# Kernel optimization log

Hardware: AMD Instinct MI355X
Metric: run time of the kernel (lower is better)

Reference implementation:

```python
import jax, jax.numpy as jnp
import numpy as np
from jax import lax

DIM = 192
HEADS = 4


def setup_inputs() -> dict:
    key = jax.random.key(0)
    ks = jax.random.split(key, 8)
    b, c, h, w = 8, DIM, 128, 128
    x = jax.random.normal(ks[0], (b, c, h, w), dtype=jnp.float32)
    Input = jax.random.normal(ks[1], (b, c, h, w), dtype=jnp.float32)
    # parameters (bias=False)
    qkv_w = jax.random.normal(ks[2], (3 * c, c), dtype=jnp.float32) * 0.02   # 1x1 conv
    dw_w = jax.random.normal(ks[3], (3 * c, 1, 3, 3), dtype=jnp.float32) * 0.02  # depthwise 3x3
    proj_w = jax.random.normal(ks[4], (c, c), dtype=jnp.float32) * 0.02      # 1x1 conv
    cm_w = jax.random.normal(ks[5], (1, c), dtype=jnp.float32) * 0.02        # changemask 1x1 conv (c -> 1)
    temperature = jnp.ones((HEADS, 1, 1), dtype=jnp.float32)
    threshold = jnp.float32(0.1)
    return {"x": x, "Input": Input, "qkv_w": qkv_w, "dw_w": dw_w,
            "proj_w": proj_w, "cm_w": cm_w, "temperature": temperature,
            "threshold": threshold}


def _l2norm(t):
    # F.normalize(dim=-1): t / max(||t||_2, eps)
    n = jnp.sqrt(jnp.sum(t * t, axis=-1, keepdims=True))
    return t / jnp.maximum(n, 1e-12)


def reference(x, Input, qkv_w, dw_w, proj_w, cm_w, temperature, threshold):
    b, c, h, w = x.shape
    # mask: threshold the residual, then a 1x1 conv to a single channel
    mask = ((Input - x) > threshold).astype(x.dtype)            # [b,c,h,w]
    mask_single = jnp.einsum('bchw,oc->bohw', mask, cm_w)        # [b,1,h,w]
    # qkv: 1x1 conv then depthwise 3x3
    qkv = jnp.einsum('bchw,oc->bohw', x, qkv_w)                  # [b,3c,h,w]
    qkv = lax.conv_general_dilated(
        qkv, dw_w, window_strides=(1, 1), padding='SAME',
        feature_group_count=3 * c,
        dimension_numbers=('NCHW', 'OIHW', 'NCHW'))
    q, k, v = jnp.split(qkv, 3, axis=1)                          # each [b,c,h,w]
    # mask repeat across channels == broadcast of single-channel mask
    q = q * mask_single
    k = k * mask_single
    ch = c // HEADS
    q = q.reshape(b, HEADS, ch, h * w)
    k = k.reshape(b, HEADS, ch, h * w)
    v = v.reshape(b, HEADS, ch, h * w)
    q = _l2norm(q)
    k = _l2norm(k)
    attn = jnp.einsum('bhcn,bhdn->bhcd', q, k) * temperature      # [b,head,ch,ch]
    attn = jax.nn.softmax(attn, axis=-1)
    out = jnp.einsum('bhcd,bhdn->bhcn', attn, v)                  # [b,head,ch,hw]
    out = out.reshape(b, c, h, w)
    out = jnp.einsum('bchw,oc->bohw', out, proj_w)                # project_out 1x1
    return out
```

## Files before the change

kernel.cpp:

```cpp
#include <hip/hip_runtime.h>
#include <hip/hip_bf16.h>

#define B 8
#define C 192
#define OC 576
#define H 128
#define W 128
#define N (H*W)
#define HEADS 4
#define CH 48

typedef __attribute__((ext_vector_type(8))) short short8;
typedef __attribute__((ext_vector_type(4))) float floatx4;

__device__ __forceinline__ float bf2f(unsigned short u) {
    union { unsigned int i; float f; } v; v.i = ((unsigned int)u) << 16; return v.f;
}
__device__ __forceinline__ unsigned short f2bf(float f) {
    __hip_bfloat16 h = (__hip_bfloat16)f;
    unsigned short u; __builtin_memcpy(&u, &h, 2); return u;
}

__global__ void k_zero(float* __restrict__ normsq, float* __restrict__ G) {
    int i = blockIdx.x * 256 + threadIdx.x;
    if (i < B * 2 * C) normsq[i] = 0.0f;
    if (i < B * HEADS * CH * CH) G[i] = 0.0f;
}

__global__ __launch_bounds__(256) void k_mask_xt(
    const float* __restrict__ x, const float* __restrict__ inp,
    const float* __restrict__ cm_w, const float* __restrict__ thr,
    float* __restrict__ mask_single, unsigned short* __restrict__ xt) {
    __shared__ unsigned short t[32][C + 2];
    __shared__ float partials[32][32];
    __shared__ float cw[C];
    int tid = threadIdx.x;
    if (tid < C) cw[tid] = cm_w[tid];
    int b = blockIdx.y, n0 = blockIdx.x * 32;
    float th = thr[0];
    const float* xb = x + (size_t)b * C * N + n0;
    const float* ib = inp + (size_t)b * C * N + n0;
    int nn4 = tid & 7;
    int c0 = tid >> 3;
    float4 xr[6], ir[6];
    #pragma unroll
    for (int it = 0; it < 6; ++it) {
        int c = c0 + it * 32;
        xr[it] = *(const float4*)&xb[(size_t)c * N + nn4 * 4];
        ir[it] = *(const float4*)&ib[(size_t)c * N + nn4 * 4];
    }
    __syncthreads();
    float s0 = 0.f, s1 = 0.f, s2 = 0.f, s3 = 0.f;
    #pragma unroll
    for (int it = 0; it < 6; ++it) {
        int c = c0 + it * 32;
        float4 xv = xr[it];
        float4 iv = ir[it];
        float wv = cw[c];
        s0 += ((iv.x - xv.x) > th) ? wv : 0.f;
        s1 += ((iv.y - xv.y) > th) ? wv : 0.f;
        s2 += ((iv.z - xv.z) > th) ? wv : 0.f;
        s3 += ((iv.w - xv.w) > th) ? wv : 0.f;
        t[nn4 * 4 + 0][c] = f2bf(xv.x);
        t[nn4 * 4 + 1][c] = f2bf(xv.y);
        t[nn4 * 4 + 2][c] = f2bf(xv.z);
        t[nn4 * 4 + 3][c] = f2bf(xv.w);
    }
    *(float4*)&partials[c0][nn4 * 4] = (float4){s0, s1, s2, s3};
    __syncthreads();
    if (tid < 32) {
        float s = 0.f;
        #pragma unroll
        for (int g = 0; g < 32; ++g) s += partials[g][tid];
        mask_single[(size_t)b * N + n0 + tid] = s;
    }
    unsigned short* db = xt + ((size_t)b * N + n0) * C;
    for (int i = tid; i < 32 * (C / 8); i += 256) {
        int r = i / (C / 8), ch = i % (C / 8);
        union { unsigned short h[8]; uint4 u; } pk;
        #pragma unroll
        for (int j = 0; j < 8; ++j) pk.h[j] = t[r][ch * 8 + j];
        *(uint4*)&db[(size_t)r * C + ch * 8] = pk.u;
    }
}

#define PAD 40
__global__ __launch_bounds__(256) void k_qkv_mfma(
    const unsigned short* __restrict__ xt, const float* __restrict__ w,
    unsigned short* __restrict__ out) {
    __shared__ __align__(16) unsigned short As[64][PAD];
    __shared__ __align__(16) unsigned short Bs[256][PAD];
    int b = blockIdx.z, m0 = blockIdx.y * 64, n0 = blockIdx.x * 256;
    int tid = threadIdx.x, wave = tid >> 6, lane = tid & 63;
    int l15 = lane & 15, quad = lane >> 4;
    floatx4 acc[4][4];
    #pragma unroll
    for (int i = 0; i < 4; ++i)
        #pragma unroll
        for (int j = 0; j < 4; ++j) acc[i][j] = (floatx4){0.f, 0.f, 0.f, 0.f};
    const unsigned short* xb = xt + (size_t)b * N * C;
    for (int k0 = 0; k0 < C; k0 += 32) {
        {
            int m = tid >> 2, ko = tid & 3;
            const float* wr = w + (size_t)(m0 + m) * C + k0 + ko * 8;
            float4 f0 = *(const float4*)&wr[0];
            float4 f1 = *(const float4*)&wr[4];
            unsigned int* dp = (unsigned int*)&As[m][ko * 8];
            dp[0] = (unsigned int)f2bf(f0.x) | ((unsigned int)f2bf(f0.y) << 16);
            dp[1] = (unsigned int)f2bf(f0.z) | ((unsigned int)f2bf(f0.w) << 16);
            dp[2] = (unsigned int)f2bf(f1.x) | ((unsigned int)f2bf(f1.y) << 16);
            dp[3] = (unsigned int)f2bf(f1.z) | ((unsigned int)f2bf(f1.w) << 16);
        }
        #pragma unroll
        for (int t = 0; t < 4; ++t) {
            int i = tid + t * 256;
            int n = i >> 2, ko = i & 3;
            *(uint4*)&Bs[n][ko * 8] = *(const uint4*)&xb[(size_t)(n0 + n) * C + k0 + ko * 8];
        }
        __syncthreads();
        short8 af[4], bf[4];
        #pragma unroll
        for (int mt = 0; mt < 4; ++mt)
            af[mt] = *(const short8*)&As[mt * 16 + l15][quad * 8];
        #pragma unroll
        for (int nt = 0; nt < 4; ++nt)
            bf[nt] = *(const short8*)&Bs[wave * 64 + nt * 16 + l15][quad * 8];
        #pragma unroll
        for (int mt = 0; mt < 4; ++mt)
            #pragma unroll
            for (int nt = 0; nt < 4; ++nt)
                acc[mt][nt] = __builtin_amdgcn_mfma_f32_16x16x32_bf16(
                    af[mt], bf[nt], acc[mt][nt], 0, 0, 0);
        __syncthreads();
    }
    unsigned short* ob = out + (size_t)b * OC * N;
    #pragma unroll
    for (int mt = 0; mt < 4; ++mt)
        #pragma unroll
        for (int r = 0; r < 4; ++r) {
            int o = m0 + mt * 16 + quad * 4 + r;
            #pragma unroll
            for (int nt = 0; nt < 4; ++nt)
                ob[(size_t)o * N + n0 + wave * 64 + nt * 16 + l15] =
                    f2bf(acc[mt][nt][r]);
        }
}

__global__ __launch_bounds__(256) void k_dwconv(
    const unsigned short* __restrict__ qkv_raw, const float* __restrict__ dw_w,
    const float* __restrict__ mask_single, unsigned short* __restrict__ qk_out,
    unsigned short* __restrict__ v_out, float* __restrict__ normsq) {
    __shared__ float tile[34][132];
    __shared__ float red[4];
    int tid = threadIdx.x;
    int b = blockIdx.z, o = blockIdx.y;
    int y0 = blockIdx.x * 32;
    const unsigned short* in = qkv_raw + ((size_t)b * OC + o) * N;
    for (int i = tid; i < 34 * 16; i += 256) {
        int r = i >> 4, dw = i & 15;
        int yy = y0 + r - 1;
        float4 f0 = {0.f, 0.f, 0.f, 0.f};
        float4 f1 = {0.f, 0.f, 0.f, 0.f};
        if (yy >= 0 && yy < H) {
            uint4 u = *(const uint4*)&in[yy * W + dw * 8];
            union { unsigned int i; float f; } a0, a1, a2, a3, a4, a5, a6, a7;
            a0.i = u.x << 16; a1.i = u.x & 0xffff0000u;
            a2.i = u.y << 16; a3.i = u.y & 0xffff0000u;
            a4.i = u.z << 16; a5.i = u.z & 0xffff0000u;
            a6.i = u.w << 16; a7.i = u.w & 0xffff0000u;
            f0.x = a0.f; f0.y = a1.f; f0.z = a2.f; f0.w = a3.f;
            f1.x = a4.f; f1.y = a5.f; f1.z = a6.f; f1.w = a7.f;
        }
        *(float4*)&tile[r][dw * 8] = f0;
        *(float4*)&tile[r][dw * 8 + 4] = f1;
        if (dw == 0)  { tile[r][130] = 0.f; tile[r][131] = 0.f; }
        if (dw == 15) { tile[r][128] = 0.f; }
    }
    __syncthreads();
    const float* wp = dw_w + o * 9;
    float w00 = wp[0], w01 = wp[1], w02 = wp[2];
    float w10 = wp[3], w11 = wp[4], w12 = wp[5];
    float w20 = wp[6], w21 = wp[7], w22 = wp[8];
    int c = tid & 63, g = tid >> 6;
    int col = c * 2;
    int lbase = (c == 0) ? 130 : (col - 2);
    bool is_qk = (o < 2 * C);
    float m_acc = 0.f;
    int rbase = g * 8;
    float2 p0l = *(const float2*)&tile[rbase][lbase];
    float2 p0m = *(const float2*)&tile[rbase][col];
    float2 p0r = *(const float2*)&tile[rbase][col + 2];
    float2 p1l = *(const float2*)&tile[rbase + 1][lbase];
    float2 p1m = *(const float2*)&tile[rbase + 1][col];
    float2 p1r = *(const float2*)&tile[rbase + 1][col + 2];
    unsigned short* qkb = qk_out + ((size_t)b * 2 * C + o) * N;
    unsigned short* vb  = v_out + ((size_t)b * C + (o - 2 * C)) * N;
    const float* mb = mask_single + (size_t)b * N;
    #pragma unroll
    for (int rl = 0; rl < 8; ++rl) {
        int tr = rbase + rl + 2;
        float2 p2l = *(const float2*)&tile[tr][lbase];
        float2 p2m = *(const float2*)&tile[tr][col];
        float2 p2r = *(const float2*)&tile[tr][col + 2];
        float sx = w00 * p0l.y + w01 * p0m.x + w02 * p0m.y
                 + w10 * p1l.y + w11 * p1m.x + w12 * p1m.y
                 + w20 * p2l.y + w21 * p2m.x + w22 * p2m.y;
        float sy = w00 * p0m.x + w01 * p0m.y + w02 * p0r.x
                 + w10 * p1m.x + w11 * p1m.y + w12 * p1r.x
                 + w20 * p2m.x + w21 * p2m.y + w22 * p2r.x;
        int p = (y0 + rbase + rl) * W + col;
        if (is_qk) {
            float2 mv = *(const float2*)&mb[p];
            sx *= mv.x; sy *= mv.y;
        }
        unsigned short hx = f2bf(sx), hy = f2bf(sy);
        unsigned int pk = (unsigned int)hx | ((unsigned int)hy << 16);
        if (is_qk) {
            *(unsigned int*)&qkb[p] = pk;
            float fx = bf2f(hx), fy = bf2f(hy);
            m_acc += fx * fx + fy * fy;
        } else {
            *(unsigned int*)&vb[p] = pk;
        }
        p0l = p1l; p0m = p1m; p0r = p1r;
        p1l = p2l; p1m = p2m; p1r = p2r;
    }
    if (is_qk) {
        #pragma unroll
        for (int off = 32; off > 0; off >>= 1) m_acc += __shfl_down(m_acc, off);
        if ((tid & 63) == 0) red[tid >> 6] = m_acc;
        __syncthreads();
        if (tid == 0)
            atomicAdd(&normsq[b * 2 * C + o], red[0] + red[1] + red[2] + red[3]);
    }
}

__global__ __launch_bounds__(256) void k_xpose_v(
    const unsigned short* __restrict__ src, unsigned short* __restrict__ dst) {
    __shared__ unsigned short t[64][C + 2];
    int tid = threadIdx.x;
    int b = blockIdx.y, n0 = blockIdx.x * 64;
    const unsigned short* sb = src + (size_t)b * C * N;
    for (int i = tid; i < C * 32; i += 256) {
        int c = i >> 5, np = i & 31;
        unsigned int u = *(const unsigned int*)&sb[(size_t)c * N + n0 + np * 2];
        t[np * 2][c] = (unsigned short)(u & 0xffffu);
        t[np * 2 + 1][c] = (unsigned short)(u >> 16);
    }
    __syncthreads();
    unsigned short* db = dst + ((size_t)b * N + n0) * C;
    for (int i = tid; i < 64 * (C / 8); i += 256) {
        int nn = i / (C / 8), ch = i % (C / 8);
        union { unsigned short h[8]; uint4 u; } pk;
        #pragma unroll
        for (int j = 0; j < 8; ++j) pk.h[j] = t[nn][ch * 8 + j];
        *(uint4*)&db[(size_t)nn * C + ch * 8] = pk.u;
    }
}

__global__ __launch_bounds__(256) void k_gram_mfma(
    const unsigned short* __restrict__ qk, float* __restrict__ G) {
    __shared__ float Gs[4][CH][CH];
    int tid = threadIdx.x, wave = tid >> 6, lane = tid & 63;
    int l15 = lane & 15, quad = lane >> 4;
    int b = blockIdx.z, hh = blockIdx.y;
    int nb = blockIdx.x * 512 + wave * 128;
    const unsigned short* qb = qk + ((size_t)b * 2 * C + hh * CH) * N;
    const unsigned short* kb = qb + (size_t)C * N;
    floatx4 acc[3][3];
    #pragma unroll
    for (int i = 0; i < 3; ++i)
        #pragma unroll
        for (int j = 0; j < 3; ++j) acc[i][j] = (floatx4){0.f, 0.f, 0.f, 0.f};
    #pragma unroll
    for (int ks = 0; ks < 4; ++ks) {
        int n_off = nb + ks * 32 + quad * 8;
        short8 af[3], bf[3];
        #pragma unroll
        for (int it = 0; it < 3; ++it)
            af[it] = *(const short8*)&qb[(size_t)(it * 16 + l15) * N + n_off];
        #pragma unroll
        for (int jt = 0; jt < 3; ++jt)
            bf[jt] = *(const short8*)&kb[(size_t)(jt * 16 + l15) * N + n_off];
        #pragma unroll
        for (int it = 0; it < 3; ++it)
            #pragma unroll
            for (int jt = 0; jt < 3; ++jt)
                acc[it][jt] = __builtin_amdgcn_mfma_f32_16x16x32_bf16(
                    af[it], bf[jt], acc[it][jt], 0, 0, 0);
    }
    #pragma unroll
    for (int it = 0; it < 3; ++it)
        #pragma unroll
        for (int jt = 0; jt < 3; ++jt)
            #pragma unroll
            for (int r = 0; r < 4; ++r)
                Gs[wave][it * 16 + quad * 4 + r][jt * 16 + l15] = acc[it][jt][r];
    __syncthreads();
    float* Gb = G + (size_t)(b * HEADS + hh) * CH * CH;
    for (int idx = tid; idx < CH * CH; idx += 256) {
        int i = idx / CH, j = idx % CH;
        atomicAdd(&Gb[idx], Gs[0][i][j] + Gs[1][i][j] + Gs[2][i][j] + Gs[3][i][j]);
    }
}

__global__ __launch_bounds__(256) void k_attn_weff(
    const float* __restrict__ G, const float* __restrict__ normsq,
    const float* __restrict__ temperature, const float* __restrict__ proj_w,
    unsigned short* __restrict__ W_eff) {
    int b = blockIdx.x;
    int o_base = blockIdx.y * 32;
    __shared__ float attn[HEADS][CH][CH];
    __shared__ float inv_n[2 * C];
    int tid = threadIdx.x;
    for (int l = tid; l < 2 * C; l += 256)
        inv_n[l] = 1.0f / fmaxf(sqrtf(normsq[b * 2 * C + l]), 1e-12f);
    __syncthreads();
    if (tid < HEADS * CH) {
        int hh = tid / CH, i = tid % CH;
        float iq = inv_n[hh * CH + i] * temperature[hh];
        const float* Gr = G + ((size_t)(b * HEADS + hh) * CH + i) * CH;
        float mx = -1e30f;
        for (int j = 0; j < CH; ++j) {
            float l2 = Gr[j] * iq * inv_n[C + hh * CH + j];
            attn[hh][i][j] = l2;
            mx = fmaxf(mx, l2);
        }
        float sm = 0.0f;
        for (int j = 0; j < CH; ++j) {
            float e = expf(attn[hh][i][j] - mx);
            attn[hh][i][j] = e;
            sm += e;
        }
        float is = 1.0f / sm;
        for (int j = 0; j < CH; ++j) attn[hh][i][j] *= is;
    }
    __syncthreads();
    for (int idx = tid; idx < 32 * C; idx += 256) {
        int o = o_base + idx / C, cp = idx % C;
        int hh = cp / CH, j = cp % CH;
        const float* pw = proj_w + (size_t)o * C + hh * CH;
        float s = 0.0f;
        #pragma unroll 8
        for (int i = 0; i < CH; ++i) s += pw[i] * attn[hh][i][j];
        W_eff[((size_t)b * C + o) * C + cp] = f2bf(s);
    }
}

__global__ __launch_bounds__(256) void k_out_mfma(
    const unsigned short* __restrict__ vt, const unsigned short* __restrict__ W_eff,
    float* __restrict__ out) {
    __shared__ __align__(16) unsigned short As[64][PAD];
    __shared__ __align__(16) unsigned short Bs[256][PAD];
    int b = blockIdx.z, m0 = blockIdx.y * 64, n0 = blockIdx.x * 256;
    int tid = threadIdx.x, wave = tid >> 6, lane = tid & 63;
    int l15 = lane & 15, quad = lane >> 4;
    floatx4 acc[4][4];
    #pragma unroll
    for (int i = 0; i < 4; ++i)
        #pragma unroll
        for (int j = 0; j < 4; ++j) acc[i][j] = (floatx4){0.f, 0.f, 0.f, 0.f};
    const unsigned short* vb = vt + (size_t)b * N * C;
    const unsigned short* wb = W_eff + (size_t)b * C * C;
    for (int k0 = 0; k0 < C; k0 += 32) {
        {
            int m = tid >> 2, ko = tid & 3;
            *(uint4*)&As[m][ko * 8] = *(const uint4*)&wb[(size_t)(m0 + m) * C + k0 + ko * 8];
        }
        #pragma unroll
        for (int t = 0; t < 4; ++t) {
            int i = tid + t * 256;
            int n = i >> 2, ko = i & 3;
            *(uint4*)&Bs[n][ko * 8] = *(const uint4*)&vb[(size_t)(n0 + n) * C + k0 + ko * 8];
        }
        __syncthreads();
        short8 af[4], bf[4];
        #pragma unroll
        for (int mt = 0; mt < 4; ++mt)
            af[mt] = *(const short8*)&As[mt * 16 + l15][quad * 8];
        #pragma unroll
        for (int nt = 0; nt < 4; ++nt)
            bf[nt] = *(const short8*)&Bs[wave * 64 + nt * 16 + l15][quad * 8];
        #pragma unroll
        for (int mt = 0; mt < 4; ++mt)
            #pragma unroll
            for (int nt = 0; nt < 4; ++nt)
                acc[mt][nt] = __builtin_amdgcn_mfma_f32_16x16x32_bf16(
                    af[mt], bf[nt], acc[mt][nt], 0, 0, 0);
        __syncthreads();
    }
    float* ob = out + (size_t)b * C * N;
    #pragma unroll
    for (int mt = 0; mt < 4; ++mt)
        #pragma unroll
        for (int r = 0; r < 4; ++r) {
            int o = m0 + mt * 16 + quad * 4 + r;
            #pragma unroll
            for (int nt = 0; nt < 4; ++nt)
                ob[(size_t)o * N + n0 + wave * 64 + nt * 16 + l15] = acc[mt][nt][r];
        }
}

extern "C" void kernel_launch(void* const* d_in, const int* in_sizes, int n_in,
                              void* d_out, int out_size, void* d_ws, size_t ws_size,
                              hipStream_t stream) {
    const float* x           = (const float*)d_in[0];
    const float* inp         = (const float*)d_in[1];
    const float* qkv_w       = (const float*)d_in[2];
    const float* dw_w        = (const float*)d_in[3];
    const float* proj_w      = (const float*)d_in[4];
    const float* cm_w        = (const float*)d_in[5];
    const float* temperature = (const float*)d_in[6];
    const float* threshold   = (const float*)d_in[7];
    float* out = (float*)d_out;

    char* ws = (char*)d_ws;
    const size_t SZ_RAW = (size_t)B * OC * N * 2;
    const size_t SZ_QK  = (size_t)B * 2 * C * N * 2;
    const size_t SZ_XT  = (size_t)B * N * C * 2;
    unsigned short* qkv_raw = (unsigned short*)ws;
    unsigned short* v_t     = (unsigned short*)ws;
    unsigned short* qk      = (unsigned short*)(ws + SZ_RAW);
    unsigned short* xt      = (unsigned short*)(ws + SZ_RAW + SZ_QK);
    unsigned short* vbuf    = xt;
    char* tail = ws + SZ_RAW + SZ_QK + SZ_XT;
    float* mask_single = (float*)tail;
    float* normsq = (float*)(tail + (size_t)B * N * 4);
    float* G = normsq + B * 2 * C;
    unsigned short* W_eff = (unsigned short*)(G + B * HEADS * CH * CH);

    k_zero<<<dim3((B * HEADS * CH * CH + 255) / 256), 256, 0, stream>>>(normsq, G);
    k_mask_xt<<<dim3(N / 32, B), 256, 0, stream>>>(x, inp, cm_w, threshold, mask_single, xt);
    k_qkv_mfma<<<dim3(N / 256, OC / 64, B), 256, 0, stream>>>(xt, qkv_w, qkv_raw);
    k_dwconv<<<dim3(H / 32, OC, B), 256, 0, stream>>>(qkv_raw, dw_w, mask_single, qk, vbuf, normsq);
    k_xpose_v<<<dim3(N / 64, B), 256, 0, stream>>>(vbuf, v_t);
    k_gram_mfma<<<dim3(N / 512, HEADS, B), 256, 0, stream>>>(qk, G);
    k_attn_weff<<<dim3(B, 6), 256, 0, stream>>>(G, normsq, temperature, proj_w, W_eff);
    k_out_mfma<<<dim3(N / 256, C / 64, B), 256, 0, stream>>>(v_t, W_eff, out);
}
```

Baseline: 509.4 us.

## Load mask/transpose tiles straight into LDS with async global_load_lds copies

The mask-and-transpose kernel now uses global-to-LDS async copies to stage fp32 x and Input tiles in shared memory, instead of loading them into registers. Each thread then reads a column of channels for one pixel, computes its share of the mask sum, and packs bf16 pairs into 16-byte stores to the transposed output. This drops the bf16 LDS transpose buffer and its second store loop, and shrinks the partial-sum reduction from 32 to 8 groups. The trade-offs are more LDS per block, which can lower occupancy, and reliance on the async copies being complete at the barrier.

```diff
diff --git a/kernel.cpp b/kernel.cpp
--- a/kernel.cpp
+++ b/kernel.cpp
@@ -21,6 +21,12 @@
     unsigned short u; __builtin_memcpy(&u, &h, 2); return u;
 }
 
+__device__ __forceinline__ void async_copy16(const float* g, float* l) {
+    __builtin_amdgcn_global_load_lds(
+        (const __attribute__((address_space(1))) unsigned int*)g,
+        (__attribute__((address_space(3))) unsigned int*)l, 16, 0, 0);
+}
+
 __global__ void k_zero(float* __restrict__ normsq, float* __restrict__ G) {
     int i = blockIdx.x * 256 + threadIdx.x;
     if (i < B * 2 * C) normsq[i] = 0.0f;
@@ -31,56 +37,50 @@
     const float* __restrict__ x, const float* __restrict__ inp,
     const float* __restrict__ cm_w, const float* __restrict__ thr,
     float* __restrict__ mask_single, unsigned short* __restrict__ xt) {
-    __shared__ unsigned short t[32][C + 2];
-    __shared__ float partials[32][32];
+    __shared__ float xs[C][32];
+    __shared__ float is_[C][32];
     __shared__ float cw[C];
+    __shared__ float partials[8][32];
     int tid = threadIdx.x;
-    if (tid < C) cw[tid] = cm_w[tid];
+    int wave = tid >> 6, lane = tid & 63;
     int b = blockIdx.y, n0 = blockIdx.x * 32;
-    float th = thr[0];
     const float* xb = x + (size_t)b * C * N + n0;
     const float* ib = inp + (size_t)b * C * N + n0;
-    int nn4 = tid & 7;
-    int c0 = tid >> 3;
-    float4 xr[6], ir[6];
-    #pragma unroll
-    for (int it = 0; it < 6; ++it) {
-        int c = c0 + it * 32;
-        xr[it] = *(const float4*)&xb[(size_t)c * N + nn4 * 4];
-        ir[it] = *(const float4*)&ib[(size_t)c * N + nn4 * 4];
-    }
-    __syncthreads();
-    float s0 = 0.f, s1 = 0.f, s2 = 0.f, s3 = 0.f;
-    #pragma unroll
-    for (int it = 0; it < 6; ++it) {
-        int c = c0 + it * 32;
-        float4 xv = xr[it];
-        float4 iv = ir[it];
-        float wv = cw[c];
-        s0 += ((iv.x - xv.x) > th) ? wv : 0.f;
-        s1 += ((iv.y - xv.y) > th) ? wv : 0.f;
-        s2 += ((iv.z - xv.z) > th) ? wv : 0.f;
-        s3 += ((iv.w - xv.w) > th) ? wv : 0.f;
-        t[nn4 * 4 + 0][c] = f2bf(xv.x);
-        t[nn4 * 4 + 1][c] = f2bf(xv.y);
-        t[nn4 * 4 + 2][c] = f2bf(xv.z);
-        t[nn4 * 4 + 3][c] = f2bf(xv.w);
-    }
-    *(float4*)&partials[c0][nn4 * 4] = (float4){s0, s1, s2, s3};
+    int cR = lane >> 3, sub = lane & 7;
+    #pragma unroll
+    for (int i = 0; i < 6; ++i) {
+        int c_base = i * 32 + wave * 8;
+        const float* gx = xb + (size_t)(c_base + cR) * N + sub * 4;
+        const float* gi = ib + (size_t)(c_base + cR) * N + sub * 4;
+        async_copy16(gx, &xs[c_base][0]);
+        async_copy16(gi, &is_[c_base][0]);
+    }
+    if (tid < C) cw[tid] = cm_w[tid];
+    float th = thr[0];
+    __syncthreads();
+    int p = tid & 31, cg = tid >> 5;
+    float macc = 0.0f;
+    unsigned int pk[12];
+    #pragma unroll
+    for (int j = 0; j < 12; ++j) {
+        int c = cg * 24 + j * 2;
+        float x0 = xs[c][p],  x1 = xs[c + 1][p];
+        float i0 = is_[c][p], i1 = is_[c + 1][p];
+        macc += ((i0 - x0) > th) ? cw[c] : 0.f;
+        macc += ((i1 - x1) > th) ? cw[c + 1] : 0.f;
+        pk[j] = (unsigned int)f2bf(x0) | ((unsigned int)f2bf(x1) << 16);
+    }
+    unsigned short* db = xt + ((size_t)b * N + n0) * C;
+    *(uint4*)&db[(size_t)p * C + cg * 24]      = *(uint4*)&pk[0];
+    *(uint4*)&db[(size_t)p * C + cg * 24 + 8]  = *(uint4*)&pk[4];
+    *(uint4*)&db[(size_t)p * C + cg * 24 + 16] = *(uint4*)&pk[8];
+    partials[cg][p] = macc;
     __syncthreads();
     if (tid < 32) {
         float s = 0.f;
         #pragma unroll
-        for (int g = 0; g < 32; ++g) s += partials[g][tid];
+        for (int g = 0; g < 8; ++g) s += partials[g][tid];
         mask_single[(size_t)b * N + n0 + tid] = s;
-    }
-    unsigned short* db = xt + ((size_t)b * N + n0) * C;
-    for (int i = tid; i < 32 * (C / 8); i += 256) {
-        int r = i / (C / 8), ch = i % (C / 8);
-        union { unsigned short h[8]; uint4 u; } pk;
-        #pragma unroll
-        for (int j = 0; j < 8; ++j) pk.h[j] = t[r][ch * 8 + j];
-        *(uint4*)&db[(size_t)r * C + ch * 8] = pk.u;
     }
 }
 
```

Result: no change. 510.3 us (+0.2%).
